# Kernel tuning notes

Measured on AMD Instinct MI355X. Metric: run time of the kernel, lower is better.

## Reference

```python
import jax, jax.numpy as jnp
import numpy as np

V, C, E, L, M = 100000, 420000, 1260000, 3, 64
FV = FC = 3
ED = 2


def _gru(x, h, wih, whh, bih, bhh):
    # PyTorch GRUCell semantics. x: [N, in], h: [N, H], wih: [3H, in], whh: [3H, H]
    gi = x @ wih.T + bih
    gh = h @ whh.T + bhh
    H = h.shape[-1]
    r = jax.nn.sigmoid(gi[:, :H] + gh[:, :H])
    z = jax.nn.sigmoid(gi[:, H:2 * H] + gh[:, H:2 * H])
    n = jnp.tanh(gi[:, 2 * H:] + r * gh[:, 2 * H:])
    return (1.0 - z) * n + z * h


def setup_inputs() -> dict:
    key = jax.random.key(0)
    ks = iter(jax.random.split(key, 40))
    f = lambda shape, s=0.1: jax.random.normal(next(ks), shape, jnp.float32) * s
    inp = {
        'var_features': jax.random.normal(next(ks), (V, FV), jnp.float32),
        'clause_features': jax.random.normal(next(ks), (C, FC), jnp.float32),
        'edge_features': jax.random.uniform(next(ks), (E, ED), dtype=jnp.float32),
        'v2c_w1': f((L, M, FV + ED)), 'v2c_b1': f((L, M)),
        'v2c_w2': f((L, M, M)), 'v2c_b2': f((L, M)),
        'c2v_w1': f((L, M, FC + ED)), 'c2v_b1': f((L, M)),
        'c2v_w2': f((L, M, M)), 'c2v_b2': f((L, M)),
        'var_gru_wih': f((L, 3 * FV, M)), 'var_gru_whh': f((L, 3 * FV, FV)),
        'var_gru_bih': f((L, 3 * FV)), 'var_gru_bhh': f((L, 3 * FV)),
        'cls_gru_wih': f((L, 3 * FC, M)), 'cls_gru_whh': f((L, 3 * FC, FC)),
        'cls_gru_bih': f((L, 3 * FC)), 'cls_gru_bhh': f((L, 3 * FC)),
        'att_w1': f((L, M, FC)), 'att_b1': f((L, M)),
        'att_w2': f((L, 1, M)), 'att_b2': f((L, 1)),
        'var_idx': jax.random.randint(next(ks), (E,), 0, V),
        'clause_idx': jax.random.randint(next(ks), (E,), 0, C),
    }
    return inp


def reference(var_features, clause_features, edge_features,
              v2c_w1, v2c_b1, v2c_w2, v2c_b2,
              c2v_w1, c2v_b1, c2v_w2, c2v_b2,
              var_gru_wih, var_gru_whh, var_gru_bih, var_gru_bhh,
              cls_gru_wih, cls_gru_whh, cls_gru_bih, cls_gru_bhh,
              att_w1, att_b1, att_w2, att_b2,
              var_idx, clause_idx):
    vf, cf = var_features, clause_features
    for l in range(L):  # fixed small number of message-passing steps
        # var -> clause: gather, edge MLP, attention-weight, scatter-add
        v2c_in = jnp.concatenate([vf[var_idx], edge_features], axis=1)  # [E, FV+ED]
        m = jnp.maximum(v2c_in @ v2c_w1[l].T + v2c_b1[l], 0.0) @ v2c_w2[l].T + v2c_b2[l]  # [E, M]
        att = (jnp.tanh(cf @ att_w1[l].T + att_b1[l]) @ att_w2[l].T + att_b2[l])[:, 0]  # [C]
        att = jax.nn.softmax(att, axis=0)
        m = m * att[clause_idx][:, None]
        cmsg = jax.ops.segment_sum(m, clause_idx, num_segments=C)  # [C, M]
        cf_new = _gru(cmsg, cf, cls_gru_wih[l], cls_gru_whh[l], cls_gru_bih[l], cls_gru_bhh[l])
        # clause -> var uses OLD clause features (matches torch forward ordering)
        c2v_in = jnp.concatenate([cf[clause_idx], edge_features], axis=1)  # [E, FC+ED]
        mv = jnp.maximum(c2v_in @ c2v_w1[l].T + c2v_b1[l], 0.0) @ c2v_w2[l].T + c2v_b2[l]  # [E, M]
        vmsg = jax.ops.segment_sum(mv, var_idx, num_segments=V)  # [V, M]
        vf = _gru(vmsg, vf, var_gru_wih[l], var_gru_whh[l], var_gru_bih[l], var_gru_bhh[l])
        cf = cf_new
    return jnp.concatenate([vf, cf], axis=0)  # [V+C, 3]
```

## Files before the change

### kernel.cpp

```cpp
#include <hip/hip_runtime.h>
#include <hip/hip_fp16.h>
#include <math.h>

#define V_N 100000
#define C_N 420000
#define E_N 1260000
#define L_N 3
#define NCBLK 1641
#define NVBLK 391
#define NEBLK 4922

__device__ __forceinline__ float fsig(float x) {
    return 1.0f / (1.0f + __expf(-x));
}
__device__ __forceinline__ float ftanh(float x) {
    x = fminf(fmaxf(x, -15.0f), 15.0f);
    float t = __expf(2.0f * x);
    return (t - 1.0f) / (t + 1.0f);
}

__global__ void k_prep(const float* __restrict__ v2c_w1, const float* __restrict__ v2c_b1,
                       const float* __restrict__ v2c_w2, const float* __restrict__ v2c_b2,
                       const float* __restrict__ c2v_w1, const float* __restrict__ c2v_b1,
                       const float* __restrict__ c2v_w2, const float* __restrict__ c2v_b2,
                       const float* __restrict__ cls_wih, const float* __restrict__ var_wih,
                       float* __restrict__ prep) {
    int t = blockIdx.x * blockDim.x + threadIdx.x;
    if (t >= 6 * 1040) return;
    int s = t / 1040, r = t % 1040;
    int side = s / 3, l = s % 3;
    const float* w1  = (side ? c2v_w1 : v2c_w1) + l * 320;
    const float* b1  = (side ? c2v_b1 : v2c_b1) + l * 64;
    const float* W2  = (side ? c2v_w2 : v2c_w2) + l * 4096;
    const float* b2  = (side ? c2v_b2 : v2c_b2) + l * 64;
    const float* wih = (side ? var_wih : cls_wih) + l * 576;
    float v = 0.0f;
    if (r < 1024) {
        int j = r >> 4, q = r & 15;
        if (q < 5) v = w1[j * 5 + q];
        else if (q == 5) v = b1[j];
        else if (q < 15) {
            int k = q - 6; float a = 0.0f;
            for (int o = 0; o < 64; ++o) a += wih[k * 64 + o] * W2[o * 64 + j];
            v = a;
        }
    } else if (r < 1033) {
        int k = r - 1024; float a = 0.0f;
        for (int o = 0; o < 64; ++o) a += wih[k * 64 + o] * b2[o];
        v = a;
    }
    prep[t] = v;
}

__global__ __launch_bounds__(256) void k_countrank(const int* __restrict__ ci,
                                                   const int* __restrict__ vi,
                                                   int* __restrict__ cntC, int* __restrict__ cntV,
                                                   int* __restrict__ rankC, int* __restrict__ rankV) {
    int e = blockIdx.x * 256 + threadIdx.x;
    if (e >= E_N) return;
    rankC[e] = atomicAdd(&cntC[ci[e]], 1);
    rankV[e] = atomicAdd(&cntV[vi[e]], 1);
}

__global__ __launch_bounds__(256) void k_scanA(const int* __restrict__ cntC,
                                               const int* __restrict__ cntV, int nbC,
                                               int* __restrict__ bsumC, int* __restrict__ bsumV) {
    int b = blockIdx.x, t = threadIdx.x;
    const int* cnt; int N; int* bs; int bb;
    if (b < nbC) { cnt = cntC; N = C_N; bs = bsumC; bb = b; }
    else         { cnt = cntV; N = V_N; bs = bsumV; bb = b - nbC; }
    int base = bb * 1024 + t * 4;
    int s = 0;
    #pragma unroll
    for (int q = 0; q < 4; ++q) { int i = base + q; if (i < N) s += cnt[i]; }
    __shared__ int sh[256];
    sh[t] = s; __syncthreads();
    for (int d = 128; d; d >>= 1) { if (t < d) sh[t] += sh[t + d]; __syncthreads(); }
    if (t == 0) bs[bb] = sh[0];
}

__global__ __launch_bounds__(512) void k_scanB(int* __restrict__ bsumC, int nbC, int* __restrict__ totC,
                                               int* __restrict__ bsumV, int nbV, int* __restrict__ totV) {
    int* bsum = blockIdx.x ? bsumV : bsumC;
    int nb    = blockIdx.x ? nbV : nbC;
    int* tot  = blockIdx.x ? totV : totC;
    __shared__ int sh[512];
    int t = threadIdx.x;
    int v = (t < nb) ? bsum[t] : 0;
    sh[t] = v; __syncthreads();
    for (int d = 1; d < 512; d <<= 1) {
        int add = (t >= d) ? sh[t - d] : 0;
        __syncthreads();
        sh[t] += add;
        __syncthreads();
    }
    if (t < nb) bsum[t] = sh[t] - v;
    if (t == nb - 1) *tot = sh[t];
}

__global__ __launch_bounds__(256) void k_scanC(const int* __restrict__ cntC,
                                               const int* __restrict__ cntV, int nbC,
                                               const int* __restrict__ bsumC,
                                               const int* __restrict__ bsumV,
                                               int* __restrict__ rowC, int* __restrict__ rowV) {
    int b = blockIdx.x, t = threadIdx.x;
    const int* cnt; int N; const int* bs; int* row; int bb;
    if (b < nbC) { cnt = cntC; N = C_N; bs = bsumC; row = rowC; bb = b; }
    else         { cnt = cntV; N = V_N; bs = bsumV; row = rowV; bb = b - nbC; }
    int base = bb * 1024 + t * 4;
    int v[4], local[4];
    #pragma unroll
    for (int q = 0; q < 4; ++q) { int i = base + q; v[q] = (i < N) ? cnt[i] : 0; }
    local[0] = 0; local[1] = v[0]; local[2] = v[0] + v[1]; local[3] = v[0] + v[1] + v[2];
    int mysum = local[3] + v[3];
    __shared__ int sh[256];
    sh[t] = mysum; __syncthreads();
    for (int d = 1; d < 256; d <<= 1) {
        int add = (t >= d) ? sh[t - d] : 0;
        __syncthreads();
        sh[t] += add;
        __syncthreads();
    }
    int excl = sh[t] - mysum + bs[bb];
    #pragma unroll
    for (int q = 0; q < 4; ++q) {
        int i = base + q;
        if (i < N) row[i] = excl + local[q];
    }
}

__global__ __launch_bounds__(256) void k_att0(const float* __restrict__ cf,
                                              const float* __restrict__ aw1,
                                              const float* __restrict__ ab1,
                                              const float* __restrict__ aw2,
                                              const float* __restrict__ ab2,
                                              float* __restrict__ logits,
                                              float* __restrict__ pmax,
                                              float* __restrict__ Sg) {
    if (blockIdx.x == 0 && threadIdx.x < 8) Sg[threadIdx.x] = 0.0f;
    int c = blockIdx.x * blockDim.x + threadIdx.x;
    float logit = -1e30f;
    if (c < C_N) {
        float h0 = cf[c * 3], h1 = cf[c * 3 + 1], h2 = cf[c * 3 + 2];
        float acc = ab2[0];
        #pragma unroll
        for (int k = 0; k < 64; ++k) {
            float tv = ftanh(aw1[k * 3] * h0 + aw1[k * 3 + 1] * h1 +
                             aw1[k * 3 + 2] * h2 + ab1[k]);
            acc += aw2[k] * tv;
        }
        logits[c] = acc;
        logit = acc;
    }
    float m = logit;
    #pragma unroll
    for (int off = 32; off; off >>= 1) m = fmaxf(m, __shfl_xor(m, off));
    __shared__ float smax[4];
    int lane = threadIdx.x & 63, wid = threadIdx.x >> 6;
    if (lane == 0) smax[wid] = m;
    __syncthreads();
    if (threadIdx.x == 0)
        pmax[blockIdx.x] = fmaxf(fmaxf(smax[0], smax[1]), fmaxf(smax[2], smax[3]));
}

__global__ __launch_bounds__(256) void k_edgeM(const float* __restrict__ vf,
                                               const float* __restrict__ cf,
                                               const float* __restrict__ ef,
                                               const int* __restrict__ var_idx,
                                               const int* __restrict__ cls_idx,
                                               const int* __restrict__ rowC,
                                               const int* __restrict__ rowV,
                                               const int* __restrict__ rankC,
                                               const int* __restrict__ rankV,
                                               const float* __restrict__ prepA,
                                               const float* __restrict__ prepB,
                                               const float* __restrict__ logits,
                                               const float* __restrict__ pmax,
                                               float* __restrict__ SgL,
                                               uint2* __restrict__ umsgC,
                                               uint2* __restrict__ umsgV) {
    __shared__ float WA[1040], WB[1040];
    for (int i = threadIdx.x; i < 1040; i += 256) { WA[i] = prepA[i]; WB[i] = prepB[i]; }
    __syncthreads();
    int e = blockIdx.x * 256 + threadIdx.x;
    if (e < E_N) {
        int v = var_idx[e], c = cls_idx[e];
        float2 efv = *(const float2*)(ef + 2 * (size_t)e);
        float a0 = vf[v * 3], a1 = vf[v * 3 + 1], a2 = vf[v * 3 + 2];
        float b0 = cf[c * 3], b1 = cf[c * 3 + 1], b2 = cf[c * 3 + 2];
        float uC[9], uV[9];
        #pragma unroll
        for (int k = 0; k < 9; ++k) { uC[k] = 0.0f; uV[k] = 0.0f; }
        for (int j = 0; j < 64; ++j) {
            const float* wj = &WA[j * 16];
            float h = fmaxf(wj[0] * a0 + wj[1] * a1 + wj[2] * a2 +
                            wj[3] * efv.x + wj[4] * efv.y + wj[5], 0.0f);
            const float* qj = &WB[j * 16];
            float g = fmaxf(qj[0] * b0 + qj[1] * b1 + qj[2] * b2 +
                            qj[3] * efv.x + qj[4] * efv.y + qj[5], 0.0f);
            #pragma unroll
            for (int k = 0; k < 9; ++k) { uC[k] += wj[6 + k] * h; uV[k] += qj[6 + k] * g; }
        }
        union { __half h[12]; uint2 q[3]; } pk;
        #pragma unroll
        for (int k = 0; k < 9; ++k) pk.h[k] = __float2half(uC[k]);
        pk.h[9] = pk.h[10] = pk.h[11] = __float2half(0.0f);
        size_t pC = (size_t)(rowC[c] + rankC[e]) * 3;
        umsgC[pC] = pk.q[0]; umsgC[pC + 1] = pk.q[1]; umsgC[pC + 2] = pk.q[2];
        #pragma unroll
        for (int k = 0; k < 9; ++k) pk.h[k] = __float2half(uV[k]);
        size_t pV = (size_t)(rowV[v] + rankV[e]) * 3;
        umsgV[pV] = pk.q[0]; umsgV[pV + 1] = pk.q[1]; umsgV[pV + 2] = pk.q[2];
    }
    if (blockIdx.x < NCBLK) {
        __shared__ float sh[4];
        float m = -1e30f;
        for (int i = threadIdx.x; i < NCBLK; i += 256) m = fmaxf(m, pmax[i]);
        #pragma unroll
        for (int off = 32; off; off >>= 1) m = fmaxf(m, __shfl_xor(m, off));
        int lane = threadIdx.x & 63, wid = threadIdx.x >> 6;
        if (lane == 0) sh[wid] = m;
        __syncthreads();
        float mm = fmaxf(fmaxf(sh[0], sh[1]), fmaxf(sh[2], sh[3]));
        __syncthreads();
        int c = blockIdx.x * 256 + threadIdx.x;
        float ex = (c < C_N) ? __expf(logits[c] - mm) : 0.0f;
        #pragma unroll
        for (int off = 32; off; off >>= 1) ex += __shfl_xor(ex, off);
        if (lane == 0) sh[wid] = ex;
        __syncthreads();
        if (threadIdx.x == 0) {
            unsafeAtomicAdd(&SgL[0], sh[0] + sh[1] + sh[2] + sh[3]);
            if (blockIdx.x == 0) SgL[1] = mm;
        }
    }
}

__global__ __launch_bounds__(256) void k_nodeM(const uint2* __restrict__ umsgC,
                                               const uint2* __restrict__ umsgV,
                                               const int* __restrict__ rowC,
                                               const int* __restrict__ rowV,
                                               const float* __restrict__ cfin,
                                               const float* __restrict__ vfin,
                                               float* __restrict__ cfout,
                                               float* __restrict__ vfout,
                                               const float* __restrict__ SgL,
                                               float* __restrict__ logits,
                                               float* __restrict__ pmax,
                                               const float* __restrict__ c2C,
                                               const float* __restrict__ c2V,
                                               const float* __restrict__ cls_whh,
                                               const float* __restrict__ cls_bih,
                                               const float* __restrict__ cls_bhh,
                                               const float* __restrict__ var_whh,
                                               const float* __restrict__ var_bih,
                                               const float* __restrict__ var_bhh,
                                               const float* __restrict__ aw1,
                                               const float* __restrict__ ab1,
                                               const float* __restrict__ aw2,
                                               const float* __restrict__ ab2,
                                               int do_att) {
    int b = blockIdx.x;
    if (b < NCBLK) {
        int i = b * 256 + threadIdx.x;
        float logit = -1e30f;
        if (i < C_N) {
            int p0 = rowC[i], p1 = rowC[i + 1];
            float u[9];
            #pragma unroll
            for (int k = 0; k < 9; ++k) u[k] = 0.0f;
            for (int p = p0; p < p1; ++p) {
                union { __half h[12]; uint2 q[3]; } pk;
                const uint2* r = umsgC + (size_t)p * 3;
                pk.q[0] = r[0]; pk.q[1] = r[1]; pk.q[2] = r[2];
                #pragma unroll
                for (int k = 0; k < 9; ++k) u[k] += __half2float(pk.h[k]);
            }
            float cnt = (float)(p1 - p0);
            float scale = __expf(logits[i] - SgL[1]) / SgL[0];
            float h0 = cfin[i * 3], h1 = cfin[i * 3 + 1], h2 = cfin[i * 3 + 2];
            float gi[9], gh[9];
            #pragma unroll
            for (int k = 0; k < 9; ++k) gi[k] = scale * (u[k] + cnt * c2C[k]) + cls_bih[k];
            #pragma unroll
            for (int k = 0; k < 9; ++k)
                gh[k] = cls_whh[k * 3] * h0 + cls_whh[k * 3 + 1] * h1 + cls_whh[k * 3 + 2] * h2 + cls_bhh[k];
            float r0 = fsig(gi[0] + gh[0]), r1 = fsig(gi[1] + gh[1]), r2 = fsig(gi[2] + gh[2]);
            float z0 = fsig(gi[3] + gh[3]), z1 = fsig(gi[4] + gh[4]), z2 = fsig(gi[5] + gh[5]);
            float n0 = ftanh(gi[6] + r0 * gh[6]);
            float n1 = ftanh(gi[7] + r1 * gh[7]);
            float n2 = ftanh(gi[8] + r2 * gh[8]);
            float o0 = (1.0f - z0) * n0 + z0 * h0;
            float o1 = (1.0f - z1) * n1 + z1 * h1;
            float o2 = (1.0f - z2) * n2 + z2 * h2;
            cfout[i * 3 + 0] = o0;
            cfout[i * 3 + 1] = o1;
            cfout[i * 3 + 2] = o2;
            if (do_att) {
                float acc = ab2[0];
                #pragma unroll
                for (int k = 0; k < 64; ++k) {
                    float tv = ftanh(aw1[k * 3] * o0 + aw1[k * 3 + 1] * o1 +
                                     aw1[k * 3 + 2] * o2 + ab1[k]);
                    acc += aw2[k] * tv;
                }
                logits[i] = acc;
                logit = acc;
            }
        }
        if (do_att) {
            float m = logit;
            #pragma unroll
            for (int off = 32; off; off >>= 1) m = fmaxf(m, __shfl_xor(m, off));
            __shared__ float smax[4];
            int lane = threadIdx.x & 63, wid = threadIdx.x >> 6;
            if (lane == 0) smax[wid] = m;
            __syncthreads();
            if (threadIdx.x == 0)
                pmax[b] = fmaxf(fmaxf(smax[0], smax[1]), fmaxf(smax[2], smax[3]));
        }
    } else {
        int i = (b - NCBLK) * 256 + threadIdx.x;
        if (i >= V_N) return;
        int p0 = rowV[i], p1 = rowV[i + 1];
        float u[9];
        #pragma unroll
        for (int k = 0; k < 9; ++k) u[k] = 0.0f;
        for (int p = p0; p < p1; ++p) {
            union { __half h[12]; uint2 q[3]; } pk;
            const uint2* r = umsgV + (size_t)p * 3;
            pk.q[0] = r[0]; pk.q[1] = r[1]; pk.q[2] = r[2];
            #pragma unroll
            for (int k = 0; k < 9; ++k) u[k] += __half2float(pk.h[k]);
        }
        float cnt = (float)(p1 - p0);
        float h0 = vfin[i * 3], h1 = vfin[i * 3 + 1], h2 = vfin[i * 3 + 2];
        float gi[9], gh[9];
        #pragma unroll
        for (int k = 0; k < 9; ++k) gi[k] = u[k] + cnt * c2V[k] + var_bih[k];
        #pragma unroll
        for (int k = 0; k < 9; ++k)
            gh[k] = var_whh[k * 3] * h0 + var_whh[k * 3 + 1] * h1 + var_whh[k * 3 + 2] * h2 + var_bhh[k];
        float r0 = fsig(gi[0] + gh[0]), r1 = fsig(gi[1] + gh[1]), r2 = fsig(gi[2] + gh[2]);
        float z0 = fsig(gi[3] + gh[3]), z1 = fsig(gi[4] + gh[4]), z2 = fsig(gi[5] + gh[5]);
        float n0 = ftanh(gi[6] + r0 * gh[6]);
        float n1 = ftanh(gi[7] + r1 * gh[7]);
        float n2 = ftanh(gi[8] + r2 * gh[8]);
        vfout[i * 3 + 0] = (1.0f - z0) * n0 + z0 * h0;
        vfout[i * 3 + 1] = (1.0f - z1) * n1 + z1 * h1;
        vfout[i * 3 + 2] = (1.0f - z2) * n2 + z2 * h2;
    }
}

extern "C" void kernel_launch(void* const* d_in, const int* in_sizes, int n_in,
                              void* d_out, int out_size, void* d_ws, size_t ws_size,
                              hipStream_t stream) {
    const float* vf0     = (const float*)d_in[0];
    const float* cf0     = (const float*)d_in[1];
    const float* ef      = (const float*)d_in[2];
    const float* v2c_w1  = (const float*)d_in[3];
    const float* v2c_b1  = (const float*)d_in[4];
    const float* v2c_w2  = (const float*)d_in[5];
    const float* v2c_b2  = (const float*)d_in[6];
    const float* c2v_w1  = (const float*)d_in[7];
    const float* c2v_b1  = (const float*)d_in[8];
    const float* c2v_w2  = (const float*)d_in[9];
    const float* c2v_b2  = (const float*)d_in[10];
    const float* var_wih = (const float*)d_in[11];
    const float* var_whh = (const float*)d_in[12];
    const float* var_bih = (const float*)d_in[13];
    const float* var_bhh = (const float*)d_in[14];
    const float* cls_wih = (const float*)d_in[15];
    const float* cls_whh = (const float*)d_in[16];
    const float* cls_bih = (const float*)d_in[17];
    const float* cls_bhh = (const float*)d_in[18];
    const float* att_w1  = (const float*)d_in[19];
    const float* att_b1  = (const float*)d_in[20];
    const float* att_w2  = (const float*)d_in[21];
    const float* att_b2  = (const float*)d_in[22];
    const int*   var_idx = (const int*)d_in[23];
    const int*   cls_idx = (const int*)d_in[24];
    float* dout = (float*)d_out;

    char* w = (char*)d_ws;
    auto alloc = [&](size_t bytes) { char* p = w; w += (bytes + 255) & ~(size_t)255; return p; };
    int*   rowC   = (int*)alloc((C_N + 1) * 4);
    int*   rowV   = (int*)alloc((V_N + 1) * 4);
    int*   cntC   = (int*)alloc((size_t)C_N * 4);
    int*   cntV   = (int*)alloc((size_t)V_N * 4);
    char*  cntEnd = w;
    int*   rankC  = (int*)alloc((size_t)E_N * 4);
    int*   rankV  = (int*)alloc((size_t)E_N * 4);
    int*   bsumC  = (int*)alloc(512 * 4);
    int*   bsumV  = (int*)alloc(512 * 4);
    float* logits = (float*)alloc((size_t)C_N * 4);
    float* pmax   = (float*)alloc(2048 * 4);
    float* Sg     = (float*)alloc(64 * 4);
    float* prep   = (float*)alloc(6 * 1040 * 4);
    uint2* umsgC  = (uint2*)alloc((size_t)E_N * 3 * 8);
    uint2* umsgV  = (uint2*)alloc((size_t)E_N * 3 * 8);
    float* vfW    = (float*)alloc((size_t)V_N * 3 * 4);
    float* cfW    = (float*)alloc((size_t)C_N * 3 * 4);

    const int nbC = (C_N + 1023) / 1024;
    const int nbV = (V_N + 1023) / 1024;

    k_prep<<<(6 * 1040 + 255) / 256, 256, 0, stream>>>(
        v2c_w1, v2c_b1, v2c_w2, v2c_b2, c2v_w1, c2v_b1, c2v_w2, c2v_b2,
        cls_wih, var_wih, prep);

    hipMemsetAsync(cntC, 0, (size_t)(cntEnd - (char*)cntC), stream);
    k_countrank<<<NEBLK, 256, 0, stream>>>(cls_idx, var_idx, cntC, cntV, rankC, rankV);
    k_scanA<<<nbC + nbV, 256, 0, stream>>>(cntC, cntV, nbC, bsumC, bsumV);
    k_scanB<<<2, 512, 0, stream>>>(bsumC, nbC, rowC + C_N, bsumV, nbV, rowV + V_N);
    k_scanC<<<nbC + nbV, 256, 0, stream>>>(cntC, cntV, nbC, bsumC, bsumV, rowC, rowV);

    k_att0<<<NCBLK, 256, 0, stream>>>(cf0, att_w1, att_b1, att_w2, att_b2,
                                      logits, pmax, Sg);

    for (int l = 0; l < L_N; ++l) {
        const float* vin = (l == 0) ? vf0 : vfW;
        const float* cin = (l == 0) ? cf0 : cfW;
        float* vout = (l == 2) ? dout : vfW;
        float* cout = (l == 2) ? (dout + (size_t)V_N * 3) : cfW;
        const float* prepA = prep + l * 1040;
        const float* prepB = prep + (3 + l) * 1040;
        int la = (l < 2) ? (l + 1) : 2;

        k_edgeM<<<NEBLK, 256, 0, stream>>>(vin, cin, ef, var_idx, cls_idx,
                                           rowC, rowV, rankC, rankV,
                                           prepA, prepB, logits, pmax,
                                           Sg + 2 * l, umsgC, umsgV);

        k_nodeM<<<NCBLK + NVBLK, 256, 0, stream>>>(umsgC, umsgV, rowC, rowV,
                                                   cin, vin, cout, vout,
                                                   Sg + 2 * l, logits, pmax,
                                                   prepA + 1024, prepB + 1024,
                                                   cls_whh + l * 27, cls_bih + l * 9, cls_bhh + l * 9,
                                                   var_whh + l * 27, var_bih + l * 9, var_bhh + l * 9,
                                                   att_w1 + la * 192, att_b1 + la * 64,
                                                   att_w2 + la * 64, att_b2 + la,
                                                   (l < 2) ? 1 : 0);
    }
}
```

Baseline: 806.3 us.

## Pre-sort edges by destination and segment-reduce messages in-block before writing sums

A one-time permute kernel packs each edge's source index, destination index and edge features into int4 records sorted by clause and by variable. The per-layer edge kernel then runs separate blocks for each direction over the sorted edges. Each block reduces runs of equal destination in shared memory and writes fp32 per-node sums, using atomics only at block-boundary segments. This removes the fp16 per-edge message buffers and the per-node CSR loop in the node kernel. In exchange it adds a per-layer memset, a permute pass, and random gathers of source features in the edge kernel.

```diff
diff --git a/kernel.cpp b/kernel.cpp
--- a/kernel.cpp
+++ b/kernel.cpp
@@ -1,5 +1,5 @@
 #include <hip/hip_runtime.h>
-#include <hip/hip_fp16.h>
+#include <limits.h>
 #include <math.h>
 
 #define V_N 100000
@@ -129,6 +129,26 @@
     }
 }
 
+__global__ __launch_bounds__(256) void k_permute(const int* __restrict__ var_idx,
+                                                 const int* __restrict__ cls_idx,
+                                                 const int* __restrict__ rankC,
+                                                 const int* __restrict__ rankV,
+                                                 const float* __restrict__ ef,
+                                                 const int* __restrict__ rowC,
+                                                 const int* __restrict__ rowV,
+                                                 int4* __restrict__ edataC,
+                                                 int4* __restrict__ edataV) {
+    int e = blockIdx.x * 256 + threadIdx.x;
+    if (e >= E_N) return;
+    int v = var_idx[e], c = cls_idx[e];
+    float2 efv = *(const float2*)(ef + 2 * (size_t)e);
+    int zx = __float_as_int(efv.x), zw = __float_as_int(efv.y);
+    int4 dC; dC.x = v; dC.y = c; dC.z = zx; dC.w = zw;
+    edataC[rowC[c] + rankC[e]] = dC;
+    int4 dV; dV.x = c; dV.y = v; dV.z = zx; dV.w = zw;
+    edataV[rowV[v] + rankV[e]] = dV;
+}
+
 __global__ __launch_bounds__(256) void k_att0(const float* __restrict__ cf,
                                               const float* __restrict__ aw1,
                                               const float* __restrict__ ab1,
@@ -163,81 +183,105 @@
         pmax[blockIdx.x] = fmaxf(fmaxf(smax[0], smax[1]), fmaxf(smax[2], smax[3]));
 }
 
-__global__ __launch_bounds__(256) void k_edgeM(const float* __restrict__ vf,
+__global__ __launch_bounds__(256) void k_edge2(const float* __restrict__ vf,
                                                const float* __restrict__ cf,
-                                               const float* __restrict__ ef,
-                                               const int* __restrict__ var_idx,
-                                               const int* __restrict__ cls_idx,
-                                               const int* __restrict__ rowC,
-                                               const int* __restrict__ rowV,
-                                               const int* __restrict__ rankC,
-                                               const int* __restrict__ rankV,
+                                               const int4* __restrict__ edataC,
+                                               const int4* __restrict__ edataV,
                                                const float* __restrict__ prepA,
                                                const float* __restrict__ prepB,
                                                const float* __restrict__ logits,
                                                const float* __restrict__ pmax,
                                                float* __restrict__ SgL,
-                                               uint2* __restrict__ umsgC,
-                                               uint2* __restrict__ umsgV) {
-    __shared__ float WA[1040], WB[1040];
-    for (int i = threadIdx.x; i < 1040; i += 256) { WA[i] = prepA[i]; WB[i] = prepB[i]; }
+                                               float* __restrict__ gsumC,
+                                               float* __restrict__ gsumV) {
+    __shared__ float W[1040];
+    __shared__ float lmsg[256 * 9];
+    __shared__ int scid[256];
+    __shared__ float sh4[4];
+    const bool sideC = blockIdx.x < NEBLK;
+    const int blk = sideC ? blockIdx.x : blockIdx.x - NEBLK;
+    const int4* __restrict__ edata = sideC ? edataC : edataV;
+    const float* __restrict__ feat = sideC ? vf : cf;
+    const float* __restrict__ prepp = sideC ? prepA : prepB;
+    float* __restrict__ gsum = sideC ? gsumC : gsumV;
+    int t = threadIdx.x;
+    for (int i = t; i < 1040; i += 256) W[i] = prepp[i];
+    int p0 = blk * 256;
+    int p = p0 + t;
+    int myc = INT_MIN;
+    float u[9];
+    int4 ed;
+    if (p < E_N) ed = edata[p];
     __syncthreads();
-    int e = blockIdx.x * 256 + threadIdx.x;
-    if (e < E_N) {
-        int v = var_idx[e], c = cls_idx[e];
-        float2 efv = *(const float2*)(ef + 2 * (size_t)e);
-        float a0 = vf[v * 3], a1 = vf[v * 3 + 1], a2 = vf[v * 3 + 2];
-        float b0 = cf[c * 3], b1 = cf[c * 3 + 1], b2 = cf[c * 3 + 2];
-        float uC[9], uV[9];
-        #pragma unroll
-        for (int k = 0; k < 9; ++k) { uC[k] = 0.0f; uV[k] = 0.0f; }
+    if (p < E_N) {
+        myc = ed.y;
+        float x0 = feat[ed.x * 3], x1 = feat[ed.x * 3 + 1], x2 = feat[ed.x * 3 + 2];
+        float x3 = __int_as_float(ed.z), x4 = __int_as_float(ed.w);
+        #pragma unroll
+        for (int k = 0; k < 9; ++k) u[k] = 0.0f;
         for (int j = 0; j < 64; ++j) {
-            const float* wj = &WA[j * 16];
-            float h = fmaxf(wj[0] * a0 + wj[1] * a1 + wj[2] * a2 +
-                            wj[3] * efv.x + wj[4] * efv.y + wj[5], 0.0f);
-            const float* qj = &WB[j * 16];
-            float g = fmaxf(qj[0] * b0 + qj[1] * b1 + qj[2] * b2 +
-                            qj[3] * efv.x + qj[4] * efv.y + qj[5], 0.0f);
-            #pragma unroll
-            for (int k = 0; k < 9; ++k) { uC[k] += wj[6 + k] * h; uV[k] += qj[6 + k] * g; }
-        }
-        union { __half h[12]; uint2 q[3]; } pk;
-        #pragma unroll
-        for (int k = 0; k < 9; ++k) pk.h[k] = __float2half(uC[k]);
-        pk.h[9] = pk.h[10] = pk.h[11] = __float2half(0.0f);
-        size_t pC = (size_t)(rowC[c] + rankC[e]) * 3;
-        umsgC[pC] = pk.q[0]; umsgC[pC + 1] = pk.q[1]; umsgC[pC + 2] = pk.q[2];
-        #pragma unroll
-        for (int k = 0; k < 9; ++k) pk.h[k] = __float2half(uV[k]);
-        size_t pV = (size_t)(rowV[v] + rankV[e]) * 3;
-        umsgV[pV] = pk.q[0]; umsgV[pV + 1] = pk.q[1]; umsgV[pV + 2] = pk.q[2];
-    }
-    if (blockIdx.x < NCBLK) {
-        __shared__ float sh[4];
+            const float* wj = &W[j * 16];
+            float h = fmaxf(wj[0] * x0 + wj[1] * x1 + wj[2] * x2 +
+                            wj[3] * x3 + wj[4] * x4 + wj[5], 0.0f);
+            #pragma unroll
+            for (int k = 0; k < 9; ++k) u[k] += wj[6 + k] * h;
+        }
+        #pragma unroll
+        for (int k = 0; k < 9; ++k) lmsg[t * 9 + k] = u[k];
+    }
+    scid[t] = myc;
+    __syncthreads();
+    if (p < E_N) {
+        bool head_any = (t == 0) || (scid[t - 1] != myc);
+        if (head_any) {
+            bool trueHead = true;
+            if (t == 0 && p0 > 0)
+                trueHead = (((const int*)edata)[(size_t)(p0 - 1) * 4 + 1] != myc);
+            float acc[9];
+            #pragma unroll
+            for (int k = 0; k < 9; ++k) acc[k] = 0.0f;
+            int j = t;
+            while (j < 256 && scid[j] == myc) {
+                #pragma unroll
+                for (int k = 0; k < 9; ++k) acc[k] += lmsg[j * 9 + k];
+                ++j;
+            }
+            bool ends = (j < 256);
+            size_t base = (size_t)myc * 9;
+            if (trueHead && ends) {
+                #pragma unroll
+                for (int k = 0; k < 9; ++k) gsum[base + k] = acc[k];
+            } else {
+                #pragma unroll
+                for (int k = 0; k < 9; ++k) unsafeAtomicAdd(&gsum[base + k], acc[k]);
+            }
+        }
+    }
+    if (sideC && blk < NCBLK) {
         float m = -1e30f;
-        for (int i = threadIdx.x; i < NCBLK; i += 256) m = fmaxf(m, pmax[i]);
+        for (int i = t; i < NCBLK; i += 256) m = fmaxf(m, pmax[i]);
         #pragma unroll
         for (int off = 32; off; off >>= 1) m = fmaxf(m, __shfl_xor(m, off));
-        int lane = threadIdx.x & 63, wid = threadIdx.x >> 6;
-        if (lane == 0) sh[wid] = m;
-        __syncthreads();
-        float mm = fmaxf(fmaxf(sh[0], sh[1]), fmaxf(sh[2], sh[3]));
-        __syncthreads();
-        int c = blockIdx.x * 256 + threadIdx.x;
+        int lane = t & 63, wid = t >> 6;
+        if (lane == 0) sh4[wid] = m;
+        __syncthreads();
+        float mm = fmaxf(fmaxf(sh4[0], sh4[1]), fmaxf(sh4[2], sh4[3]));
+        __syncthreads();
+        int c = blk * 256 + t;
         float ex = (c < C_N) ? __expf(logits[c] - mm) : 0.0f;
         #pragma unroll
         for (int off = 32; off; off >>= 1) ex += __shfl_xor(ex, off);
-        if (lane == 0) sh[wid] = ex;
-        __syncthreads();
-        if (threadIdx.x == 0) {
-            unsafeAtomicAdd(&SgL[0], sh[0] + sh[1] + sh[2] + sh[3]);
-            if (blockIdx.x == 0) SgL[1] = mm;
-        }
-    }
-}
-
-__global__ __launch_bounds__(256) void k_nodeM(const uint2* __restrict__ umsgC,
-                                               const uint2* __restrict__ umsgV,
+        if (lane == 0) sh4[wid] = ex;
+        __syncthreads();
+        if (t == 0) {
+            unsafeAtomicAdd(&SgL[0], sh4[0] + sh4[1] + sh4[2] + sh4[3]);
+            if (blk == 0) SgL[1] = mm;
+        }
+    }
+}
+
+__global__ __launch_bounds__(256) void k_nodeM(const float* __restrict__ gsumC,
+                                               const float* __restrict__ gsumV,
                                                const int* __restrict__ rowC,
                                                const int* __restrict__ rowV,
                                                const float* __restrict__ cfin,
@@ -265,18 +309,10 @@
         int i = b * 256 + threadIdx.x;
         float logit = -1e30f;
         if (i < C_N) {
-            int p0 = rowC[i], p1 = rowC[i + 1];
             float u[9];
             #pragma unroll
-            for (int k = 0; k < 9; ++k) u[k] = 0.0f;
-            for (int p = p0; p < p1; ++p) {
-                union { __half h[12]; uint2 q[3]; } pk;
-                const uint2* r = umsgC + (size_t)p * 3;
-                pk.q[0] = r[0]; pk.q[1] = r[1]; pk.q[2] = r[2];
-                #pragma unroll
-                for (int k = 0; k < 9; ++k) u[k] += __half2float(pk.h[k]);
-            }
-            float cnt = (float)(p1 - p0);
+            for (int k = 0; k < 9; ++k) u[k] = gsumC[(size_t)i * 9 + k];
+            float cnt = (float)(rowC[i + 1] - rowC[i]);
             float scale = __expf(logits[i] - SgL[1]) / SgL[0];
             float h0 = cfin[i * 3], h1 = cfin[i * 3 + 1], h2 = cfin[i * 3 + 2];
             float gi[9], gh[9];
@@ -322,18 +358,10 @@
     } else {
         int i = (b - NCBLK) * 256 + threadIdx.x;
         if (i >= V_N) return;
-        int p0 = rowV[i], p1 = rowV[i + 1];
         float u[9];
         #pragma unroll
-        for (int k = 0; k < 9; ++k) u[k] = 0.0f;
-        for (int p = p0; p < p1; ++p) {
-            union { __half h[12]; uint2 q[3]; } pk;
-            const uint2* r = umsgV + (size_t)p * 3;
-            pk.q[0] = r[0]; pk.q[1] = r[1]; pk.q[2] = r[2];
-            #pragma unroll
-            for (int k = 0; k < 9; ++k) u[k] += __half2float(pk.h[k]);
-        }
-        float cnt = (float)(p1 - p0);
+        for (int k = 0; k < 9; ++k) u[k] = gsumV[(size_t)i * 9 + k];
+        float cnt = (float)(rowV[i + 1] - rowV[i]);
         float h0 = vfin[i * 3], h1 = vfin[i * 3 + 1], h2 = vfin[i * 3 + 2];
         float gi[9], gh[9];
         #pragma unroll
@@ -397,13 +425,17 @@
     float* pmax   = (float*)alloc(2048 * 4);
     float* Sg     = (float*)alloc(64 * 4);
     float* prep   = (float*)alloc(6 * 1040 * 4);
-    uint2* umsgC  = (uint2*)alloc((size_t)E_N * 3 * 8);
-    uint2* umsgV  = (uint2*)alloc((size_t)E_N * 3 * 8);
+    int4*  edataC = (int4*)alloc((size_t)E_N * 16);
+    int4*  edataV = (int4*)alloc((size_t)E_N * 16);
+    float* gsumC  = (float*)alloc((size_t)C_N * 9 * 4);
+    float* gsumV  = (float*)alloc((size_t)V_N * 9 * 4);
+    char*  gsumEnd = w;
     float* vfW    = (float*)alloc((size_t)V_N * 3 * 4);
     float* cfW    = (float*)alloc((size_t)C_N * 3 * 4);
 
     const int nbC = (C_N + 1023) / 1024;
     const int nbV = (V_N + 1023) / 1024;
+    const size_t gsum_bytes = (size_t)gsumEnd - (size_t)gsumC;
 
     k_prep<<<(6 * 1040 + 255) / 256, 256, 0, stream>>>(
         v2c_w1, v2c_b1, v2c_w2, v2c_b2, c2v_w1, c2v_b1, c2v_w2, c2v_b2,
@@ -414,6 +446,8 @@
     k_scanA<<<nbC + nbV, 256, 0, stream>>>(cntC, cntV, nbC, bsumC, bsumV);
     k_scanB<<<2, 512, 0, stream>>>(bsumC, nbC, rowC + C_N, bsumV, nbV, rowV + V_N);
     k_scanC<<<nbC + nbV, 256, 0, stream>>>(cntC, cntV, nbC, bsumC, bsumV, rowC, rowV);
+    k_permute<<<NEBLK, 256, 0, stream>>>(var_idx, cls_idx, rankC, rankV, ef,
+                                         rowC, rowV, edataC, edataV);
 
     k_att0<<<NCBLK, 256, 0, stream>>>(cf0, att_w1, att_b1, att_w2, att_b2,
                                       logits, pmax, Sg);
@@ -427,12 +461,13 @@
         const float* prepB = prep + (3 + l) * 1040;
         int la = (l < 2) ? (l + 1) : 2;
 
-        k_edgeM<<<NEBLK, 256, 0, stream>>>(vin, cin, ef, var_idx, cls_idx,
-                                           rowC, rowV, rankC, rankV,
-                                           prepA, prepB, logits, pmax,
-                                           Sg + 2 * l, umsgC, umsgV);
-
-        k_nodeM<<<NCBLK + NVBLK, 256, 0, stream>>>(umsgC, umsgV, rowC, rowV,
+        hipMemsetAsync(gsumC, 0, gsum_bytes, stream);
+
+        k_edge2<<<2 * NEBLK, 256, 0, stream>>>(vin, cin, edataC, edataV,
+                                               prepA, prepB, logits, pmax,
+                                               Sg + 2 * l, gsumC, gsumV);
+
+        k_nodeM<<<NCBLK + NVBLK, 256, 0, stream>>>(gsumC, gsumV, rowC, rowV,
                                                    cin, vin, cout, vout,
                                                    Sg + 2 * l, logits, pmax,
                                                    prepA + 1024, prepB + 1024,
```

Measured after the change: 874.7 us. 1.08x slower.
